# Kernel tuning notes

Hardware: AMD Instinct MI355X
Metric: run time of the kernel (lower is better)

Reference implementation:

```python
import jax, jax.numpy as jnp
import numpy as np

B, S, D = 4, 2048, 1024
H, DQK, DV = 16, 20, 64
DLQ, DLKV = 256, 128
EPS = 1e-6
NEG = -1e9


def _rms(x, w, eps=EPS):
    return x * jax.lax.rsqrt(jnp.mean(x * x, axis=-1, keepdims=True) + eps) * w


def setup_inputs() -> dict:
    key = jax.random.key(0)
    ks = jax.random.split(key, 12)
    sd = lambda n: 1.0 / np.sqrt(n)
    inp = {
        'h': jax.random.normal(ks[0], (B, S, D), jnp.float32),
        'mask': jnp.where(jnp.tril(jnp.ones((S, S), bool)), 0.0, NEG).astype(jnp.float32),
        'wq_a_w': jax.random.normal(ks[1], (DLQ, D), jnp.float32) * sd(D),
        'wq_a_b': jnp.zeros((DLQ,), jnp.float32),
        'q_norm_w': jnp.ones((DLQ,), jnp.float32),
        'wq_b_w': jax.random.normal(ks[2], (H * DQK, DLQ), jnp.float32) * sd(DLQ),
        'wq_b_b': jnp.zeros((H * DQK,), jnp.float32),
        'wkv_a_w': jax.random.normal(ks[3], (DLKV, D), jnp.float32) * sd(D),
        'wkv_a_b': jnp.zeros((DLKV,), jnp.float32),
        'kv_norm_w': jnp.ones((DLKV,), jnp.float32),
        'wkv_b_w': jax.random.normal(ks[4], (H * (DQK + DV), DLKV), jnp.float32) * sd(DLKV),
        'wo_w': jax.random.normal(ks[5], (D, H * DV), jnp.float32) * sd(H * DV),
        'wo_b': jnp.zeros((D,), jnp.float32),
    }
    return inp


def reference(h, mask, wq_a_w, wq_a_b, q_norm_w, wq_b_w, wq_b_b,
              wkv_a_w, wkv_a_b, kv_norm_w, wkv_b_w, wo_w, wo_b):
    b, s, _ = h.shape
    # query path: wq_b(q_norm(wq_a(h)))
    q_lat = _rms(h @ wq_a_w.T + wq_a_b, q_norm_w)
    q = (q_lat @ wq_b_w.T + wq_b_b).reshape(b, s, H, DQK)
    # latent kv (prefill, start_pos=0 => cache[:end_pos] == kv_norm of this chunk)
    kvn = _rms(h @ wkv_a_w.T + wkv_a_b, kv_norm_w)  # [b, t, c]
    wkv_b = wkv_b_w.reshape(H, DQK + DV, DLKV)
    # absorbed QK: project query into latent space
    q_kv = jnp.einsum('bshq,hqc->bshc', q, wkv_b[:, :DQK])
    scores = jnp.einsum('bshc,btc->bsht', q_kv, kvn) * (DQK ** -0.5)
    scores = scores + mask[:, None, :]  # causal, broadcast over heads
    p = jax.nn.softmax(scores, axis=-1).astype(h.dtype)
    v_lat = jnp.einsum('bsht,btc->bshc', p, kvn)
    v = jnp.einsum('bshc,hvc->bshv', v_lat, wkv_b[:, DQK:])
    return v.reshape(b, s, H * DV) @ wo_w.T + wo_b
```

## Files before the change

kernel.cpp:

```cpp
#include <hip/hip_runtime.h>
#include <stdint.h>

#define NB 4
#define SEQ 2048
#define DM 1024
#define NH 16
#define NDQK 20
#define NDV 64
#define DLQ 256
#define DLKV 128
#define MR (NB*SEQ)
#define NKV (NH*DLKV)

typedef __attribute__((ext_vector_type(8))) short bf8;
typedef __attribute__((ext_vector_type(4))) float f4;
typedef __attribute__((ext_vector_type(4))) short s4;

#define MFMA16(a,b,c) __builtin_amdgcn_mfma_f32_16x16x32_bf16(a, b, c, 0, 0, 0)

__device__ __forceinline__ short f2b(float f) {
  union { float f; unsigned u; } v; v.f = f;
  return (short)((v.u + 0x7FFFu + ((v.u >> 16) & 1u)) >> 16);
}

__device__ __forceinline__ void gld16(void* lds, const void* g) {
  __builtin_amdgcn_global_load_lds((const __attribute__((address_space(1))) void*)g,
                                   (__attribute__((address_space(3))) void*)lds, 16, 0, 0);
}

__device__ __forceinline__ float dppmax16(float v) {
  int t;
  t = __builtin_amdgcn_update_dpp(0, __float_as_int(v), 0xB1,  0xF, 0xF, true); v = fmaxf(v, __int_as_float(t));
  t = __builtin_amdgcn_update_dpp(0, __float_as_int(v), 0x4E,  0xF, 0xF, true); v = fmaxf(v, __int_as_float(t));
  t = __builtin_amdgcn_update_dpp(0, __float_as_int(v), 0x141, 0xF, 0xF, true); v = fmaxf(v, __int_as_float(t));
  t = __builtin_amdgcn_update_dpp(0, __float_as_int(v), 0x140, 0xF, 0xF, true); v = fmaxf(v, __int_as_float(t));
  return v;
}

__global__ __launch_bounds__(256) void k_conv(const float* __restrict__ h,
    const float* __restrict__ wqa, const float* __restrict__ wkva,
    short* __restrict__ hb, short* __restrict__ wqab, short* __restrict__ wkvab) {
  const int NH4 = (MR*DM)/4, NQ4 = (DLQ*DM)/4, NK4 = (DLKV*DM)/4;
  int stride = gridDim.x * blockDim.x;
  for (int i = blockIdx.x*blockDim.x + threadIdx.x; i < NH4+NQ4+NK4; i += stride) {
    const float4* s; short* d; int o;
    if (i < NH4)            { s = (const float4*)h;    d = hb;     o = i; }
    else if (i < NH4+NQ4)   { s = (const float4*)wqa;  d = wqab;   o = i - NH4; }
    else                    { s = (const float4*)wkva; d = wkvab;  o = i - NH4 - NQ4; }
    float4 v = s[o];
    s4 r; r.x = f2b(v.x); r.y = f2b(v.y); r.z = f2b(v.z); r.w = f2b(v.w);
    *(s4*)(d + (size_t)o*4) = r;
  }
}

__global__ __launch_bounds__(256) void k_wcomb(const float* __restrict__ wqbw,
    const float* __restrict__ wqbb, const float* __restrict__ wkvb,
    short* __restrict__ Wc, float* __restrict__ bc) {
  const float SC = 0.22360679774997896f * 1.4426950408889634f;
  int n = blockIdx.x, l = threadIdx.x;
  int hh = n >> 7, c = n & 127;
  float acc = 0.f, bacc = 0.f;
  for (int q = 0; q < NDQK; ++q) {
    float wv = wkvb[(hh*84 + q)*128 + c];
    acc  += wqbw[(hh*20 + q)*256 + l] * wv;
    bacc += wqbb[hh*20 + q] * wv;
  }
  Wc[(size_t)n*256 + l] = f2b(acc * SC);
  if (l == 0) bc[n] = bacc * SC;
}

__global__ __launch_bounds__(256) void k_w2(const float* __restrict__ wo,
    const float* __restrict__ wkvb, short* __restrict__ W2) {
  int idx = blockIdx.x*256 + threadIdx.x;
  int d = idx >> 11, k = idx & 2047, hh = k >> 7, c = k & 127;
  float acc = 0.f;
  #pragma unroll 8
  for (int v = 0; v < NDV; ++v)
    acc += wo[d*1024 + hh*64 + v] * wkvb[(hh*84 + 20 + v)*128 + c];
  W2[idx] = f2b(acc);
}

template<int BN, bool WT>
__global__ __launch_bounds__(256) void k_proj_rms(const short* __restrict__ Ab,
    const short* __restrict__ Wb, const float* __restrict__ bias,
    const float* __restrict__ nw, short* __restrict__ outp, short* __restrict__ outT) {
  constexpr int WN = BN/4, NI = WN/16;
  __shared__ __align__(16) char As[32*128];
  __shared__ __align__(16) char Ws[BN*128];
  __shared__ float red[32][4];
  const int tid = threadIdx.x, l = tid & 63, w = tid >> 6;
  const int l15 = l & 15, l4 = l >> 4, l7 = l & 7, l3 = l >> 3;
  const int m0 = blockIdx.x * 32;
  f4 z = {0.f,0.f,0.f,0.f};
  f4 acc[2][NI];
  for (int mi=0;mi<2;mi++) for (int ni=0;ni<NI;ni++) acc[mi][ni] = z;
  for (int kt = 0; kt < DM/64; ++kt) {
    __syncthreads();
    { int row = w*8 + l3;
      gld16(As + w*1024 + l*16,
            (const char*)Ab + ((size_t)(m0+row)*DM + kt*64)*2 + ((l7 ^ (row&7))*16)); }
    #pragma unroll
    for (int i = 0; i < BN/32; ++i) {
      int ci = w*(BN/32) + i, row = ci*8 + l3;
      gld16(Ws + ci*1024 + l*16,
            (const char*)Wb + ((size_t)row*DM + kt*64)*2 + ((l7 ^ (row&7))*16));
    }
    asm volatile("s_waitcnt vmcnt(0)" ::: "memory");
    __syncthreads();
    #pragma unroll
    for (int kk = 0; kk < 2; ++kk) {
      bf8 a[2], bb[NI];
      #pragma unroll
      for (int mi=0;mi<2;mi++) { int row = mi*16 + l15;
        a[mi] = *(const bf8*)(As + row*128 + ((kk*64 + l4*16) ^ ((row&7)<<4))); }
      #pragma unroll
      for (int ni=0;ni<NI;ni++) { int n = w*WN + ni*16 + l15;
        bb[ni] = *(const bf8*)(Ws + n*128 + ((kk*64 + l4*16) ^ ((n&7)<<4))); }
      #pragma unroll
      for (int mi=0;mi<2;mi++)
        #pragma unroll
        for (int ni=0;ni<NI;ni++) acc[mi][ni] = MFMA16(a[mi], bb[ni], acc[mi][ni]);
    }
  }
  float bn[NI], nwv[NI];
  #pragma unroll
  for (int ni=0;ni<NI;ni++) { int n = w*WN + ni*16 + l15; bn[ni] = bias[n]; nwv[ni] = nw[n]; }
  #pragma unroll
  for (int mi=0;mi<2;mi++) {
    f4 v = z;
    #pragma unroll
    for (int ni=0;ni<NI;ni++)
      #pragma unroll
      for (int r=0;r<4;r++) { acc[mi][ni][r] += bn[ni]; v[r] += acc[mi][ni][r]*acc[mi][ni][r]; }
    #pragma unroll
    for (int r=0;r<4;r++)
      for (int x=1;x<16;x<<=1) v[r] += __shfl_xor(v[r], x);
    if (l15 == 0) {
      #pragma unroll
      for (int r=0;r<4;r++) red[mi*16 + l4*4 + r][w] = v[r];
    }
  }
  __syncthreads();
  #pragma unroll
  for (int mi=0;mi<2;mi++) {
    float sc[4];
    #pragma unroll
    for (int r=0;r<4;r++) { int row = mi*16 + l4*4 + r;
      float t = red[row][0] + red[row][1] + red[row][2] + red[row][3];
      sc[r] = rsqrtf(t * (1.0f/BN) + 1e-6f); }
    #pragma unroll
    for (int ni=0;ni<NI;ni++) { int n = w*WN + ni*16 + l15;
      #pragma unroll
      for (int r=0;r<4;r++) {
        int m = m0 + mi*16 + l4*4 + r;
        short bv = f2b(acc[mi][ni][r] * sc[r] * nwv[ni]);
        outp[(size_t)m*BN + n] = bv;
        if (WT) { int bb2 = m >> 11, s = m & 2047;
                  outT[((size_t)bb2*DLKV + n)*SEQ + s] = bv; }
      }
    }
  }
}

template<bool BOUT>
__global__ __launch_bounds__(256) void k_gemm(const short* __restrict__ A,
    const short* __restrict__ W, const float* __restrict__ bias,
    void* __restrict__ outp, int N, int K) {
  __shared__ __align__(16) char As[128*128];
  __shared__ __align__(16) char Ws[128*128];
  const int tid = threadIdx.x, l = tid & 63, w = tid >> 6;
  const int l15 = l&15, l4 = l>>4, l7 = l&7, l3 = l>>3;
  const int wm = w >> 1, wn = w & 1;
  const int n0 = blockIdx.x * 128, m0 = blockIdx.y * 128;
  f4 z = {0.f,0.f,0.f,0.f};
  f4 acc[4][4];
  for (int mi=0;mi<4;mi++) for (int ni=0;ni<4;ni++) acc[mi][ni] = z;
  for (int kt = 0; kt < (K>>6); ++kt) {
    __syncthreads();
    #pragma unroll
    for (int i=0;i<4;i++) {
      int ci = w*4 + i, row = ci*8 + l3;
      gld16(As + ci*1024 + l*16,
            (const char*)A + ((size_t)(m0+row)*K + kt*64)*2 + ((l7^(row&7))*16));
      gld16(Ws + ci*1024 + l*16,
            (const char*)W + ((size_t)(n0+row)*K + kt*64)*2 + ((l7^(row&7))*16));
    }
    asm volatile("s_waitcnt vmcnt(0)" ::: "memory");
    __syncthreads();
    #pragma unroll
    for (int kk=0;kk<2;kk++) {
      bf8 a[4], bb[4];
      #pragma unroll
      for (int mi=0;mi<4;mi++) { int row = wm*64+mi*16+l15;
        a[mi] = *(const bf8*)(As + row*128 + ((kk*64+l4*16)^((row&7)<<4))); }
      #pragma unroll
      for (int ni=0;ni<4;ni++) { int row = wn*64+ni*16+l15;
        bb[ni] = *(const bf8*)(Ws + row*128 + ((kk*64+l4*16)^((row&7)<<4))); }
      #pragma unroll
      for (int mi=0;mi<4;mi++)
        #pragma unroll
        for (int ni=0;ni<4;ni++) acc[mi][ni] = MFMA16(a[mi], bb[ni], acc[mi][ni]);
    }
  }
  #pragma unroll
  for (int ni=0;ni<4;ni++) {
    int n = n0 + wn*64 + ni*16 + l15;
    float bn = bias[n];
    #pragma unroll
    for (int mi=0;mi<4;mi++)
      #pragma unroll
      for (int r=0;r<4;r++) {
        int m = m0 + wm*64 + mi*16 + l4*4 + r;
        float val = acc[mi][ni][r] + bn;
        if (BOUT) ((short*)outp)[(size_t)m*N + n] = f2b(val);
        else      ((float*)outp)[(size_t)m*N + n] = val;
      }
  }
}

__global__ __launch_bounds__(512, 1) void k_flash(const short* __restrict__ qkv,
    const short* __restrict__ kvn, const short* __restrict__ kvnT,
    short* __restrict__ vlat) {
  __shared__ __align__(16) char Ks[2][64*256];
  __shared__ __align__(16) short Pl[8][32*72];
  const int tid = threadIdx.x, l = tid & 63, w = tid >> 6;
  const int l15 = l & 15, l4 = l >> 4;
  const int id = blockIdx.x;
  const int b   = (id & 7) >> 1;
  const int hh  = (((id >> 3) & 1) << 3) | w;
  const int y   = ((id >> 4) << 1) | (id & 1);
  const int qbs0 = y, qbs1 = 63 - y;
  const int ntA = (y >> 1) + 1, ntT = 33;
  const short* Kb = kvn  + (size_t)b*SEQ*DLKV;
  const short* Vb = kvnT + (size_t)b*DLKV*SEQ;
  short* Pw = Pl[w];

  const short ONE = 0x3F80;
  bf8 ones;
  #pragma unroll
  for (int j2=0;j2<8;j2++) ones[j2] = ONE;
  f4 z = {0.f,0.f,0.f,0.f};

  int qw = qbs0*32;
  size_t rowbase = (size_t)b*SEQ + qw;
  bf8 qf[2][4];
  f4 acc[2][8], sums[2]; float mr[2][4];
  #pragma unroll
  for (int mi=0;mi<2;mi++) {
    #pragma unroll
    for (int kk=0;kk<4;kk++)
      qf[mi][kk] = *(const bf8*)(qkv + (rowbase + mi*16 + l15)*NKV + hh*128 + kk*32 + l4*8);
    sums[mi] = z;
    #pragma unroll
    for (int cf=0;cf<8;cf++) acc[mi][cf] = z;
    #pragma unroll
    for (int r=0;r<4;r++) mr[mi][r] = -3.0e38f;
  }

  #pragma unroll
  for (int r=0;r<2;r++) {
    int ci = r*512 + tid, row = ci >> 4, c16 = ci & 15;
    gld16(Ks[0] + ci*16, (const char*)Kb + row*256 + ((c16 ^ (row & 7))*16));
  }
  int cur = 0, t = 0;
  for (int j = 0; j < ntT; ++j) {
    const int tn = (j+1 >= ntT) ? t : ((j+1 == ntA) ? 0 : t+1);
    {
      const char* src = (const char*)(Kb + (size_t)tn*64*DLKV);
      #pragma unroll
      for (int r=0;r<2;r++) {
        int ci = r*512 + tid, row = ci >> 4, c16 = ci & 15;
        gld16(Ks[cur^1] + ci*16, src + row*256 + ((c16 ^ (row & 7))*16));
      }
    }
    asm volatile("s_waitcnt vmcnt(2)" ::: "memory");
    __syncthreads();
    const int t0 = t*64;
    const char* kb = Ks[cur];
    f4 sc[2][4];
    #pragma unroll
    for (int mi=0;mi<2;mi++)
      #pragma unroll
      for (int tf=0;tf<4;tf++) sc[mi][tf] = z;
    #pragma unroll
    for (int kk=0;kk<4;kk++) {
      bf8 bk[4];
      #pragma unroll
      for (int tf=0;tf<4;tf++) { int tt = tf*16 + l15;
        bk[tf] = *(const bf8*)(kb + tt*256 + ((kk*64 + l4*16) ^ ((tt&7)<<4))); }
      #pragma unroll
      for (int mi=0;mi<2;mi++)
        #pragma unroll
        for (int tf=0;tf<4;tf++) sc[mi][tf] = MFMA16(qf[mi][kk], bk[tf], sc[mi][tf]);
    }
    bf8 vr0[8], vr1[8];
    #pragma unroll
    for (int cf=0;cf<8;cf++)
      vr0[cf] = *(const bf8*)(Vb + (size_t)(cf*16 + l15)*SEQ + t0 + l4*8);
    if (t0 + 63 > qw) {
      #pragma unroll
      for (int mi=0;mi<2;mi++)
        #pragma unroll
        for (int tf=0;tf<4;tf++)
          #pragma unroll
          for (int r=0;r<4;r++) {
            int qg = qw + mi*16 + l4*4 + r, tg = t0 + tf*16 + l15;
            if (tg > qg) sc[mi][tf][r] = -3.0e38f;
          }
    }
    #pragma unroll
    for (int mi=0;mi<2;mi++) {
      float mn[4], al[4];
      #pragma unroll
      for (int r=0;r<4;r++) {
        float v = fmaxf(fmaxf(sc[mi][0][r], sc[mi][1][r]), fmaxf(sc[mi][2][r], sc[mi][3][r]));
        v = dppmax16(v);
        float m2 = fmaxf(mr[mi][r], v);
        al[r] = exp2f(mr[mi][r] - m2);
        mr[mi][r] = m2; mn[r] = m2;
      }
      #pragma unroll
      for (int r=0;r<4;r++) { sums[mi][r] *= al[r];
        #pragma unroll
        for (int cf=0;cf<8;cf++) acc[mi][cf][r] *= al[r]; }
      #pragma unroll
      for (int tf=0;tf<4;tf++)
        #pragma unroll
        for (int r=0;r<4;r++)
          Pw[(mi*16 + l4*4 + r)*72 + tf*16 + l15] = f2b(exp2f(sc[mi][tf][r] - mn[r]));
    }
    #pragma unroll
    for (int cf=0;cf<8;cf++)
      vr1[cf] = *(const bf8*)(Vb + (size_t)(cf*16 + l15)*SEQ + t0 + 32 + l4*8);
    #pragma unroll
    for (int kk=0;kk<2;kk++) {
      bf8 pa[2];
      #pragma unroll
      for (int mi=0;mi<2;mi++)
        pa[mi] = *(const bf8*)(Pw + (mi*16 + l15)*72 + kk*32 + l4*8);
      #pragma unroll
      for (int mi=0;mi<2;mi++) sums[mi] = MFMA16(pa[mi], ones, sums[mi]);
      #pragma unroll
      for (int cf=0;cf<8;cf++) {
        bf8 bv = kk ? vr1[cf] : vr0[cf];
        #pragma unroll
        for (int mi=0;mi<2;mi++) acc[mi][cf] = MFMA16(pa[mi], bv, acc[mi][cf]);
      }
    }
    __syncthreads();
    cur ^= 1;
    if (j+1 == ntA || j+1 == ntT) {
      #pragma unroll
      for (int mi=0;mi<2;mi++) {
        float inv[4];
        #pragma unroll
        for (int r=0;r<4;r++) inv[r] = 1.0f / sums[mi][r];
        #pragma unroll
        for (int cf=0;cf<8;cf++)
          #pragma unroll
          for (int r=0;r<4;r++) {
            size_t m = rowbase + mi*16 + l4*4 + r;
            vlat[m*NKV + hh*128 + cf*16 + l15] = f2b(acc[mi][cf][r] * inv[r]);
          }
      }
      if (j+1 == ntA) {
        qw = qbs1*32; rowbase = (size_t)b*SEQ + qw;
        #pragma unroll
        for (int mi=0;mi<2;mi++) {
          #pragma unroll
          for (int kk=0;kk<4;kk++)
            qf[mi][kk] = *(const bf8*)(qkv + (rowbase + mi*16 + l15)*NKV + hh*128 + kk*32 + l4*8);
          sums[mi] = z;
          #pragma unroll
          for (int cf=0;cf<8;cf++) acc[mi][cf] = z;
          #pragma unroll
          for (int r=0;r<4;r++) mr[mi][r] = -3.0e38f;
        }
      }
    }
    t = tn;
  }
}

extern "C" void kernel_launch(void* const* d_in, const int* in_sizes, int n_in,
                              void* d_out, int out_size, void* d_ws, size_t ws_size,
                              hipStream_t stream) {
  const float* h     = (const float*)d_in[0];
  const float* wqaw  = (const float*)d_in[2];
  const float* wqa_b = (const float*)d_in[3];
  const float* qnw   = (const float*)d_in[4];
  const float* wqbw  = (const float*)d_in[5];
  const float* wqbb  = (const float*)d_in[6];
  const float* wkvaw = (const float*)d_in[7];
  const float* wkva_b= (const float*)d_in[8];
  const float* kvnw  = (const float*)d_in[9];
  const float* wkvb  = (const float*)d_in[10];
  const float* wow   = (const float*)d_in[11];
  const float* wob   = (const float*)d_in[12];

  char* ws = (char*)d_ws;
  size_t off = 0;
  auto alloc = [&](size_t bytes) { char* p = ws + off; off += (bytes + 255) & ~(size_t)255; return p; };
  short* hb     = (short*)alloc((size_t)MR*DM*2);
  short* wqab16 = (short*)alloc((size_t)DLQ*DM*2);
  short* wkvab16= (short*)alloc((size_t)DLKV*DM*2);
  short* qlat   = (short*)alloc((size_t)MR*DLQ*2);
  short* kvnb   = (short*)alloc((size_t)MR*DLKV*2);
  short* kvnT   = (short*)alloc((size_t)MR*DLKV*2);
  short* Wc     = (short*)alloc((size_t)NKV*DLQ*2);
  float* bc     = (float*)alloc((size_t)NKV*4);
  short* qkv    = (short*)alloc((size_t)MR*NKV*2);
  short* vlat   = (short*)alloc((size_t)MR*NKV*2);
  short* W2     = (short*)alloc((size_t)DM*NKV*2);

  k_conv<<<2048, 256, 0, stream>>>(h, wqaw, wkvaw, hb, wqab16, wkvab16);
  k_wcomb<<<NKV, 256, 0, stream>>>(wqbw, wqbb, wkvb, Wc, bc);
  k_w2<<<(DM*NKV)/256, 256, 0, stream>>>(wow, wkvb, W2);
  k_proj_rms<DLQ,  false><<<MR/32, 256, 0, stream>>>(hb, wqab16,  wqa_b,  qnw,  qlat, nullptr);
  k_proj_rms<DLKV, true ><<<MR/32, 256, 0, stream>>>(hb, wkvab16, wkva_b, kvnw, kvnb, kvnT);
  k_gemm<true ><<<dim3(NKV/128, MR/128), 256, 0, stream>>>(qlat, Wc, bc, qkv, NKV, DLQ);
  k_flash<<<256, 512, 0, stream>>>(qkv, kvnb, kvnT, vlat);
  k_gemm<false><<<dim3(DM/128, MR/128), 256, 0, stream>>>(vlat, W2, wob, d_out, DM, NKV);
}
```

Baseline: 413.0 us.

## Split flash work to 16 query rows per wave and add lazy rescaling

The flash attention kernel now gives each wave 16 query rows instead of 32. Each block holds 4 heads with two row halves instead of 8 heads, and the grid doubles to 512 blocks. Launch bounds are raised to allow 4 blocks per CU, which trades per-wave K/V reuse for occupancy and latency hiding. It also skips the online-softmax rescale of acc and sums unless some row max grows by more than 8 in log2 units, which saves VALU work but lets the unnormalized values grow.

```diff
diff --git a/kernel.cpp b/kernel.cpp
--- a/kernel.cpp
+++ b/kernel.cpp
@@ -218,17 +218,19 @@
   }
 }
 
-__global__ __launch_bounds__(512, 1) void k_flash(const short* __restrict__ qkv,
+__global__ __launch_bounds__(512, 4) void k_flash(const short* __restrict__ qkv,
     const short* __restrict__ kvn, const short* __restrict__ kvnT,
     short* __restrict__ vlat) {
   __shared__ __align__(16) char Ks[2][64*256];
-  __shared__ __align__(16) short Pl[8][32*72];
+  __shared__ __align__(16) short Pl[8][16*72];
   const int tid = threadIdx.x, l = tid & 63, w = tid >> 6;
   const int l15 = l & 15, l4 = l >> 4;
   const int id = blockIdx.x;
   const int b   = (id & 7) >> 1;
-  const int hh  = (((id >> 3) & 1) << 3) | w;
-  const int y   = ((id >> 4) << 1) | (id & 1);
+  const int u   = ((id >> 3) << 1) | (id & 1);
+  const int hg  = u & 3, y = u >> 2;
+  const int hh  = hg*4 + (w & 3);
+  const int half = w >> 2;
   const int qbs0 = y, qbs1 = 63 - y;
   const int ntA = (y >> 1) + 1, ntT = 33;
   const short* Kb = kvn  + (size_t)b*SEQ*DLKV;
@@ -241,21 +243,18 @@
   for (int j2=0;j2<8;j2++) ones[j2] = ONE;
   f4 z = {0.f,0.f,0.f,0.f};
 
-  int qw = qbs0*32;
+  int qw = qbs0*32 + half*16;
   size_t rowbase = (size_t)b*SEQ + qw;
-  bf8 qf[2][4];
-  f4 acc[2][8], sums[2]; float mr[2][4];
-  #pragma unroll
-  for (int mi=0;mi<2;mi++) {
-    #pragma unroll
-    for (int kk=0;kk<4;kk++)
-      qf[mi][kk] = *(const bf8*)(qkv + (rowbase + mi*16 + l15)*NKV + hh*128 + kk*32 + l4*8);
-    sums[mi] = z;
-    #pragma unroll
-    for (int cf=0;cf<8;cf++) acc[mi][cf] = z;
-    #pragma unroll
-    for (int r=0;r<4;r++) mr[mi][r] = -3.0e38f;
-  }
+  bf8 qf[4];
+  f4 acc[8], sums; float mr[4];
+  #pragma unroll
+  for (int kk=0;kk<4;kk++)
+    qf[kk] = *(const bf8*)(qkv + (rowbase + l15)*NKV + hh*128 + kk*32 + l4*8);
+  sums = z;
+  #pragma unroll
+  for (int cf=0;cf<8;cf++) acc[cf] = z;
+  #pragma unroll
+  for (int r=0;r<4;r++) mr[r] = -3.0e38f;
 
   #pragma unroll
   for (int r=0;r<2;r++) {
@@ -277,11 +276,9 @@
     __syncthreads();
     const int t0 = t*64;
     const char* kb = Ks[cur];
-    f4 sc[2][4];
-    #pragma unroll
-    for (int mi=0;mi<2;mi++)
-      #pragma unroll
-      for (int tf=0;tf<4;tf++) sc[mi][tf] = z;
+    f4 sc[4];
+    #pragma unroll
+    for (int tf=0;tf<4;tf++) sc[tf] = z;
     #pragma unroll
     for (int kk=0;kk<4;kk++) {
       bf8 bk[4];
@@ -289,9 +286,7 @@
       for (int tf=0;tf<4;tf++) { int tt = tf*16 + l15;
         bk[tf] = *(const bf8*)(kb + tt*256 + ((kk*64 + l4*16) ^ ((tt&7)<<4))); }
       #pragma unroll
-      for (int mi=0;mi<2;mi++)
-        #pragma unroll
-        for (int tf=0;tf<4;tf++) sc[mi][tf] = MFMA16(qf[mi][kk], bk[tf], sc[mi][tf]);
+      for (int tf=0;tf<4;tf++) sc[tf] = MFMA16(qf[kk], bk[tf], sc[tf]);
     }
     bf8 vr0[8], vr1[8];
     #pragma unroll
@@ -299,83 +294,72 @@
       vr0[cf] = *(const bf8*)(Vb + (size_t)(cf*16 + l15)*SEQ + t0 + l4*8);
     if (t0 + 63 > qw) {
       #pragma unroll
-      for (int mi=0;mi<2;mi++)
-        #pragma unroll
-        for (int tf=0;tf<4;tf++)
-          #pragma unroll
-          for (int r=0;r<4;r++) {
-            int qg = qw + mi*16 + l4*4 + r, tg = t0 + tf*16 + l15;
-            if (tg > qg) sc[mi][tf][r] = -3.0e38f;
-          }
-    }
-    #pragma unroll
-    for (int mi=0;mi<2;mi++) {
-      float mn[4], al[4];
+      for (int tf=0;tf<4;tf++)
+        #pragma unroll
+        for (int r=0;r<4;r++) {
+          int qg = qw + l4*4 + r, tg = t0 + tf*16 + l15;
+          if (tg > qg) sc[tf][r] = -3.0e38f;
+        }
+    }
+    float pmax[4];
+    #pragma unroll
+    for (int r=0;r<4;r++) {
+      float v = fmaxf(fmaxf(sc[0][r], sc[1][r]), fmaxf(sc[2][r], sc[3][r]));
+      pmax[r] = dppmax16(v);
+    }
+    bool need = false;
+    #pragma unroll
+    for (int r=0;r<4;r++) need = need || (pmax[r] > mr[r] + 8.0f);
+    if (__any(need)) {
       #pragma unroll
       for (int r=0;r<4;r++) {
-        float v = fmaxf(fmaxf(sc[mi][0][r], sc[mi][1][r]), fmaxf(sc[mi][2][r], sc[mi][3][r]));
-        v = dppmax16(v);
-        float m2 = fmaxf(mr[mi][r], v);
-        al[r] = exp2f(mr[mi][r] - m2);
-        mr[mi][r] = m2; mn[r] = m2;
+        float m2 = fmaxf(mr[r], pmax[r]);
+        float al = exp2f(mr[r] - m2);
+        mr[r] = m2;
+        sums[r] *= al;
+        #pragma unroll
+        for (int cf=0;cf<8;cf++) acc[cf][r] *= al;
       }
-      #pragma unroll
-      for (int r=0;r<4;r++) { sums[mi][r] *= al[r];
-        #pragma unroll
-        for (int cf=0;cf<8;cf++) acc[mi][cf][r] *= al[r]; }
-      #pragma unroll
-      for (int tf=0;tf<4;tf++)
-        #pragma unroll
-        for (int r=0;r<4;r++)
-          Pw[(mi*16 + l4*4 + r)*72 + tf*16 + l15] = f2b(exp2f(sc[mi][tf][r] - mn[r]));
-    }
+    }
+    #pragma unroll
+    for (int tf=0;tf<4;tf++)
+      #pragma unroll
+      for (int r=0;r<4;r++)
+        Pw[(l4*4 + r)*72 + tf*16 + l15] = f2b(exp2f(sc[tf][r] - mr[r]));
     #pragma unroll
     for (int cf=0;cf<8;cf++)
       vr1[cf] = *(const bf8*)(Vb + (size_t)(cf*16 + l15)*SEQ + t0 + 32 + l4*8);
     #pragma unroll
     for (int kk=0;kk<2;kk++) {
-      bf8 pa[2];
-      #pragma unroll
-      for (int mi=0;mi<2;mi++)
-        pa[mi] = *(const bf8*)(Pw + (mi*16 + l15)*72 + kk*32 + l4*8);
-      #pragma unroll
-      for (int mi=0;mi<2;mi++) sums[mi] = MFMA16(pa[mi], ones, sums[mi]);
-      #pragma unroll
-      for (int cf=0;cf<8;cf++) {
-        bf8 bv = kk ? vr1[cf] : vr0[cf];
-        #pragma unroll
-        for (int mi=0;mi<2;mi++) acc[mi][cf] = MFMA16(pa[mi], bv, acc[mi][cf]);
-      }
+      bf8 pa = *(const bf8*)(Pw + l15*72 + kk*32 + l4*8);
+      sums = MFMA16(pa, ones, sums);
+      #pragma unroll
+      for (int cf=0;cf<8;cf++)
+        acc[cf] = MFMA16(pa, kk ? vr1[cf] : vr0[cf], acc[cf]);
     }
     __syncthreads();
     cur ^= 1;
     if (j+1 == ntA || j+1 == ntT) {
-      #pragma unroll
-      for (int mi=0;mi<2;mi++) {
-        float inv[4];
-        #pragma unroll
-        for (int r=0;r<4;r++) inv[r] = 1.0f / sums[mi][r];
-        #pragma unroll
-        for (int cf=0;cf<8;cf++)
-          #pragma unroll
-          for (int r=0;r<4;r++) {
-            size_t m = rowbase + mi*16 + l4*4 + r;
-            vlat[m*NKV + hh*128 + cf*16 + l15] = f2b(acc[mi][cf][r] * inv[r]);
-          }
-      }
+      float inv[4];
+      #pragma unroll
+      for (int r=0;r<4;r++) inv[r] = 1.0f / sums[r];
+      #pragma unroll
+      for (int cf=0;cf<8;cf++)
+        #pragma unroll
+        for (int r=0;r<4;r++) {
+          size_t m = rowbase + l4*4 + r;
+          vlat[m*NKV + hh*128 + cf*16 + l15] = f2b(acc[cf][r] * inv[r]);
+        }
       if (j+1 == ntA) {
-        qw = qbs1*32; rowbase = (size_t)b*SEQ + qw;
-        #pragma unroll
-        for (int mi=0;mi<2;mi++) {
-          #pragma unroll
-          for (int kk=0;kk<4;kk++)
-            qf[mi][kk] = *(const bf8*)(qkv + (rowbase + mi*16 + l15)*NKV + hh*128 + kk*32 + l4*8);
-          sums[mi] = z;
-          #pragma unroll
-          for (int cf=0;cf<8;cf++) acc[mi][cf] = z;
-          #pragma unroll
-          for (int r=0;r<4;r++) mr[mi][r] = -3.0e38f;
-        }
+        qw = qbs1*32 + half*16; rowbase = (size_t)b*SEQ + qw;
+        #pragma unroll
+        for (int kk=0;kk<4;kk++)
+          qf[kk] = *(const bf8*)(qkv + (rowbase + l15)*NKV + hh*128 + kk*32 + l4*8);
+        sums = z;
+        #pragma unroll
+        for (int cf=0;cf<8;cf++) acc[cf] = z;
+        #pragma unroll
+        for (int r=0;r<4;r++) mr[r] = -3.0e38f;
       }
     }
     t = tn;
@@ -419,6 +403,6 @@
   k_proj_rms<DLQ,  false><<<MR/32, 256, 0, stream>>>(hb, wqab16,  wqa_b,  qnw,  qlat, nullptr);
   k_proj_rms<DLKV, true ><<<MR/32, 256, 0, stream>>>(hb, wkvab16, wkva_b, kvnw, kvnb, kvnT);
   k_gemm<true ><<<dim3(NKV/128, MR/128), 256, 0, stream>>>(qlat, Wc, bc, qkv, NKV, DLQ);
-  k_flash<<<256, 512, 0, stream>>>(qkv, kvnb, kvnT, vlat);
+  k_flash<<<512, 512, 0, stream>>>(qkv, kvnb, kvnT, vlat);
   k_gemm<false><<<dim3(DM/128, MR/128), 256, 0, stream>>>(vlat, W2, wob, d_out, DM, NKV);
 }
```

After: 663.0 us. +60.5%, slower.

## Restructure flash attention: transposed scores, lazy rescale, smaller blocks, packed bf16

Applied to the files above, without the earlier changes.

The flash kernel now computes transposed score tiles (K as the A operand), so each lane holds a full query row's scores and the row max needs only two cross-lane shuffles instead of DPP reductions. Accumulator rescaling is skipped unless the new max exceeds the running max by more than 8, P is packed with v_cvt_pk_bf16_f32, and V fragments are loaded just before use instead of being prefetched into registers. Blocks shrink from 512 threads with 8 heads to 256 threads with 4 heads, with a 3-blocks-per-CU launch bound and twice as many blocks, to raise occupancy. The lazy rescale risks fp32/bf16 overflow headroom and adds a shuffle per rescale, and dropping the V prefetch can expose global load latency.

```diff
diff --git a/kernel.cpp b/kernel.cpp
--- a/kernel.cpp
+++ b/kernel.cpp
@@ -15,6 +15,7 @@
 typedef __attribute__((ext_vector_type(8))) short bf8;
 typedef __attribute__((ext_vector_type(4))) float f4;
 typedef __attribute__((ext_vector_type(4))) short s4;
+typedef __attribute__((ext_vector_type(2))) unsigned int u2;
 
 #define MFMA16(a,b,c) __builtin_amdgcn_mfma_f32_16x16x32_bf16(a, b, c, 0, 0, 0)
 
@@ -23,18 +24,13 @@
   return (short)((v.u + 0x7FFFu + ((v.u >> 16) & 1u)) >> 16);
 }
 
+__device__ __forceinline__ unsigned cvtpk(float lo, float hi) {
+  unsigned d; asm("v_cvt_pk_bf16_f32 %0, %1, %2" : "=v"(d) : "v"(lo), "v"(hi)); return d;
+}
+
 __device__ __forceinline__ void gld16(void* lds, const void* g) {
   __builtin_amdgcn_global_load_lds((const __attribute__((address_space(1))) void*)g,
                                    (__attribute__((address_space(3))) void*)lds, 16, 0, 0);
-}
-
-__device__ __forceinline__ float dppmax16(float v) {
-  int t;
-  t = __builtin_amdgcn_update_dpp(0, __float_as_int(v), 0xB1,  0xF, 0xF, true); v = fmaxf(v, __int_as_float(t));
-  t = __builtin_amdgcn_update_dpp(0, __float_as_int(v), 0x4E,  0xF, 0xF, true); v = fmaxf(v, __int_as_float(t));
-  t = __builtin_amdgcn_update_dpp(0, __float_as_int(v), 0x141, 0xF, 0xF, true); v = fmaxf(v, __int_as_float(t));
-  t = __builtin_amdgcn_update_dpp(0, __float_as_int(v), 0x140, 0xF, 0xF, true); v = fmaxf(v, __int_as_float(t));
-  return v;
 }
 
 __global__ __launch_bounds__(256) void k_conv(const float* __restrict__ h,
@@ -218,22 +214,23 @@
   }
 }
 
-__global__ __launch_bounds__(512, 1) void k_flash(const short* __restrict__ qkv,
+__global__ __launch_bounds__(256, 3) void k_flash(const short* __restrict__ qkv,
     const short* __restrict__ kvn, const short* __restrict__ kvnT,
     short* __restrict__ vlat) {
   __shared__ __align__(16) char Ks[2][64*256];
-  __shared__ __align__(16) short Pl[8][32*72];
+  __shared__ __align__(16) short Pl[4][32*72];
   const int tid = threadIdx.x, l = tid & 63, w = tid >> 6;
-  const int l15 = l & 15, l4 = l >> 4;
+  const int l15 = l & 15, p = l >> 4;
   const int id = blockIdx.x;
   const int b   = (id & 7) >> 1;
-  const int hh  = (((id >> 3) & 1) << 3) | w;
-  const int y   = ((id >> 4) << 1) | (id & 1);
+  const int u   = ((id >> 3) << 1) | (id & 1);
+  const int hg  = u & 3, y = u >> 2;
+  const int hh  = hg*4 + w;
   const int qbs0 = y, qbs1 = 63 - y;
   const int ntA = (y >> 1) + 1, ntT = 33;
   const short* Kb = kvn  + (size_t)b*SEQ*DLKV;
   const short* Vb = kvnT + (size_t)b*DLKV*SEQ;
-  short* Pw = Pl[w];
+  char* Pw = (char*)Pl[w];
 
   const short ONE = 0x3F80;
   bf8 ones;
@@ -244,22 +241,21 @@
   int qw = qbs0*32;
   size_t rowbase = (size_t)b*SEQ + qw;
   bf8 qf[2][4];
-  f4 acc[2][8], sums[2]; float mr[2][4];
+  f4 acc[2][8], sums[2]; float mr[2];
   #pragma unroll
   for (int mi=0;mi<2;mi++) {
     #pragma unroll
     for (int kk=0;kk<4;kk++)
-      qf[mi][kk] = *(const bf8*)(qkv + (rowbase + mi*16 + l15)*NKV + hh*128 + kk*32 + l4*8);
+      qf[mi][kk] = *(const bf8*)(qkv + (rowbase + mi*16 + l15)*NKV + hh*128 + kk*32 + p*8);
     sums[mi] = z;
     #pragma unroll
     for (int cf=0;cf<8;cf++) acc[mi][cf] = z;
-    #pragma unroll
-    for (int r=0;r<4;r++) mr[mi][r] = -3.0e38f;
-  }
-
-  #pragma unroll
-  for (int r=0;r<2;r++) {
-    int ci = r*512 + tid, row = ci >> 4, c16 = ci & 15;
+    mr[mi] = -3.0e38f;
+  }
+
+  #pragma unroll
+  for (int r=0;r<4;r++) {
+    int ci = r*256 + tid, row = ci >> 4, c16 = ci & 15;
     gld16(Ks[0] + ci*16, (const char*)Kb + row*256 + ((c16 ^ (row & 7))*16));
   }
   int cur = 0, t = 0;
@@ -268,12 +264,12 @@
     {
       const char* src = (const char*)(Kb + (size_t)tn*64*DLKV);
       #pragma unroll
-      for (int r=0;r<2;r++) {
-        int ci = r*512 + tid, row = ci >> 4, c16 = ci & 15;
+      for (int r=0;r<4;r++) {
+        int ci = r*256 + tid, row = ci >> 4, c16 = ci & 15;
         gld16(Ks[cur^1] + ci*16, src + row*256 + ((c16 ^ (row & 7))*16));
       }
     }
-    asm volatile("s_waitcnt vmcnt(2)" ::: "memory");
+    asm volatile("s_waitcnt vmcnt(4)" ::: "memory");
     __syncthreads();
     const int t0 = t*64;
     const char* kb = Ks[cur];
@@ -287,62 +283,74 @@
       bf8 bk[4];
       #pragma unroll
       for (int tf=0;tf<4;tf++) { int tt = tf*16 + l15;
-        bk[tf] = *(const bf8*)(kb + tt*256 + ((kk*64 + l4*16) ^ ((tt&7)<<4))); }
+        bk[tf] = *(const bf8*)(kb + tt*256 + ((kk*64 + p*16) ^ ((tt&7)<<4))); }
       #pragma unroll
       for (int mi=0;mi<2;mi++)
         #pragma unroll
-        for (int tf=0;tf<4;tf++) sc[mi][tf] = MFMA16(qf[mi][kk], bk[tf], sc[mi][tf]);
-    }
-    bf8 vr0[8], vr1[8];
-    #pragma unroll
-    for (int cf=0;cf<8;cf++)
-      vr0[cf] = *(const bf8*)(Vb + (size_t)(cf*16 + l15)*SEQ + t0 + l4*8);
+        for (int tf=0;tf<4;tf++) sc[mi][tf] = MFMA16(bk[tf], qf[mi][kk], sc[mi][tf]);
+    }
     if (t0 + 63 > qw) {
       #pragma unroll
-      for (int mi=0;mi<2;mi++)
+      for (int mi=0;mi<2;mi++) {
+        int qg = qw + mi*16 + l15;
         #pragma unroll
         for (int tf=0;tf<4;tf++)
           #pragma unroll
           for (int r=0;r<4;r++) {
-            int qg = qw + mi*16 + l4*4 + r, tg = t0 + tf*16 + l15;
+            int tg = t0 + tf*16 + 4*p + r;
             if (tg > qg) sc[mi][tf][r] = -3.0e38f;
           }
-    }
+      }
+    }
+    float pmax[2];
     #pragma unroll
     for (int mi=0;mi<2;mi++) {
-      float mn[4], al[4];
-      #pragma unroll
-      for (int r=0;r<4;r++) {
-        float v = fmaxf(fmaxf(sc[mi][0][r], sc[mi][1][r]), fmaxf(sc[mi][2][r], sc[mi][3][r]));
-        v = dppmax16(v);
-        float m2 = fmaxf(mr[mi][r], v);
-        al[r] = exp2f(mr[mi][r] - m2);
-        mr[mi][r] = m2; mn[r] = m2;
-      }
-      #pragma unroll
-      for (int r=0;r<4;r++) { sums[mi][r] *= al[r];
-        #pragma unroll
-        for (int cf=0;cf<8;cf++) acc[mi][cf][r] *= al[r]; }
+      float v = -3.0e38f;
       #pragma unroll
       for (int tf=0;tf<4;tf++)
         #pragma unroll
-        for (int r=0;r<4;r++)
-          Pw[(mi*16 + l4*4 + r)*72 + tf*16 + l15] = f2b(exp2f(sc[mi][tf][r] - mn[r]));
-    }
-    #pragma unroll
-    for (int cf=0;cf<8;cf++)
-      vr1[cf] = *(const bf8*)(Vb + (size_t)(cf*16 + l15)*SEQ + t0 + 32 + l4*8);
+        for (int r=0;r<4;r++) v = fmaxf(v, sc[mi][tf][r]);
+      v = fmaxf(v, __shfl_xor(v, 16));
+      v = fmaxf(v, __shfl_xor(v, 32));
+      pmax[mi] = v;
+    }
+    bool need = (pmax[0] > mr[0] + 8.0f) || (pmax[1] > mr[1] + 8.0f);
+    if (__any(need)) {
+      #pragma unroll
+      for (int mi=0;mi<2;mi++) {
+        float m2 = fmaxf(mr[mi], pmax[mi]);
+        float al = exp2f(mr[mi] - m2);
+        mr[mi] = m2;
+        #pragma unroll
+        for (int r=0;r<4;r++) {
+          float alq = __shfl(al, (l & 48) + (p << 2) + r);
+          sums[mi][r] *= alq;
+          #pragma unroll
+          for (int cf=0;cf<8;cf++) acc[mi][cf][r] *= alq;
+        }
+      }
+    }
+    #pragma unroll
+    for (int mi=0;mi<2;mi++) {
+      #pragma unroll
+      for (int tf=0;tf<4;tf++) {
+        unsigned d0 = cvtpk(exp2f(sc[mi][tf][0] - mr[mi]), exp2f(sc[mi][tf][1] - mr[mi]));
+        unsigned d1 = cvtpk(exp2f(sc[mi][tf][2] - mr[mi]), exp2f(sc[mi][tf][3] - mr[mi]));
+        u2 dd; dd.x = d0; dd.y = d1;
+        *(u2*)(Pw + (mi*16 + l15)*144 + tf*32 + p*8) = dd;
+      }
+    }
     #pragma unroll
     for (int kk=0;kk<2;kk++) {
       bf8 pa[2];
       #pragma unroll
       for (int mi=0;mi<2;mi++)
-        pa[mi] = *(const bf8*)(Pw + (mi*16 + l15)*72 + kk*32 + l4*8);
+        pa[mi] = *(const bf8*)(Pw + (mi*16 + l15)*144 + kk*64 + p*16);
       #pragma unroll
       for (int mi=0;mi<2;mi++) sums[mi] = MFMA16(pa[mi], ones, sums[mi]);
       #pragma unroll
       for (int cf=0;cf<8;cf++) {
-        bf8 bv = kk ? vr1[cf] : vr0[cf];
+        bf8 bv = *(const bf8*)(Vb + (size_t)(cf*16 + l15)*SEQ + t0 + kk*32 + p*8);
         #pragma unroll
         for (int mi=0;mi<2;mi++) acc[mi][cf] = MFMA16(pa[mi], bv, acc[mi][cf]);
       }
@@ -359,7 +367,7 @@
         for (int cf=0;cf<8;cf++)
           #pragma unroll
           for (int r=0;r<4;r++) {
-            size_t m = rowbase + mi*16 + l4*4 + r;
+            size_t m = rowbase + mi*16 + 4*p + r;
             vlat[m*NKV + hh*128 + cf*16 + l15] = f2b(acc[mi][cf][r] * inv[r]);
           }
       }
@@ -369,12 +377,11 @@
         for (int mi=0;mi<2;mi++) {
           #pragma unroll
           for (int kk=0;kk<4;kk++)
-            qf[mi][kk] = *(const bf8*)(qkv + (rowbase + mi*16 + l15)*NKV + hh*128 + kk*32 + l4*8);
+            qf[mi][kk] = *(const bf8*)(qkv + (rowbase + mi*16 + l15)*NKV + hh*128 + kk*32 + p*8);
           sums[mi] = z;
           #pragma unroll
           for (int cf=0;cf<8;cf++) acc[mi][cf] = z;
-          #pragma unroll
-          for (int r=0;r<4;r++) mr[mi][r] = -3.0e38f;
+          mr[mi] = -3.0e38f;
         }
       }
     }
@@ -419,6 +426,6 @@
   k_proj_rms<DLQ,  false><<<MR/32, 256, 0, stream>>>(hb, wqab16,  wqa_b,  qnw,  qlat, nullptr);
   k_proj_rms<DLKV, true ><<<MR/32, 256, 0, stream>>>(hb, wkvab16, wkva_b, kvnw, kvnb, kvnT);
   k_gemm<true ><<<dim3(NKV/128, MR/128), 256, 0, stream>>>(qlat, Wc, bc, qkv, NKV, DLQ);
-  k_flash<<<256, 512, 0, stream>>>(qkv, kvnb, kvnT, vlat);
+  k_flash<<<512, 256, 0, stream>>>(qkv, kvnb, kvnT, vlat);
   k_gemm<false><<<dim3(DM/128, MR/128), 256, 0, stream>>>(vlat, W2, wob, d_out, DM, NKV);
 }
```

Result: slower. 570.8 us (+38.2%).
